# Optimization experiments

Measured on AMD Instinct MI355X. Metric: run time of the kernel, lower is better.

Reference implementation:

```python
import jax, jax.numpy as jnp
import numpy as np

B, C, N, Fd = 8, 64, 256, 128
EPS = 1e-5


def setup_inputs() -> dict:
    key = jax.random.key(0)
    k_h, k_op, k_s, k_q = jax.random.split(key, 4)
    # xavier_uniform bound for [C, 2F, 1] slices: gain*sqrt(6/(fan_in+fan_out)) with fan_in=2F, fan_out=1
    bound = float(np.sqrt(6.0 / (2 * Fd + 1)))
    h = jax.random.normal(k_h, (B, C, N, Fd), dtype=jnp.float32)
    op = jax.random.uniform(k_op, (C, 2 * Fd, 1), minval=-bound, maxval=bound, dtype=jnp.float32)
    op_S = jax.random.uniform(k_s, (C, 2 * Fd, 1), minval=-bound, maxval=bound, dtype=jnp.float32)
    op_Q = jax.random.uniform(k_q, (C, 2 * Fd, 1), minval=-bound, maxval=bound, dtype=jnp.float32)
    gamma = jnp.ones((C,), dtype=jnp.float32)
    beta = jnp.zeros((C,), dtype=jnp.float32)
    return {"h": h, "op": op, "op_S": op_S, "op_Q": op_Q, "gamma": gamma, "beta": beta}


def reference(h, op, op_S, op_Q, gamma, beta):
    # h: [B, C, N, F]
    source = h[:, :, 0:1, :]                              # [B,C,1,F]
    h_src = jnp.broadcast_to(source, h.shape)             # repeat_interleave over N
    h_op = jnp.concatenate([h_src, h], axis=-1)           # [B,C,N,2F]
    # [B,C,N,2F] x [C,2F,1] -> [B,C,N,1]
    attn_op = jax.nn.sigmoid(jnp.einsum('bcnf,cfo->bcno', h_op, op))
    op_mask = (attn_op >= 0.5).astype(h.dtype)            # hard threshold (no grad)
    supp = h * op_mask                                    # [B,C,N,F]
    query = h * (1.0 - op_mask)
    supp_mean = jnp.mean(supp, axis=2, keepdims=True)     # [B,C,1,F]
    query_mean = jnp.mean(query, axis=2, keepdims=True)
    supp_attn = jnp.einsum('bcnf,cfo->bcno', jnp.concatenate([supp_mean, source], axis=-1), op_S)
    query_attn = jnp.einsum('bcnf,cfo->bcno', jnp.concatenate([query_mean, source], axis=-1), op_Q)
    op_attn = jax.nn.softmax(jnp.concatenate([supp_attn, query_attn], axis=-1), axis=-1)  # [B,C,1,2]
    h_opn = supp * op_attn[..., 0:1] + query * op_attn[..., 1:2]  # [B,C,N,F]
    # BatchNorm2d (training-mode batch stats) over (B,N,F) per channel
    mean = jnp.mean(h_opn, axis=(0, 2, 3), keepdims=True)
    var = jnp.var(h_opn, axis=(0, 2, 3), keepdims=True)
    h_bn = (h_opn - mean) * jax.lax.rsqrt(var + EPS)
    h_bn = h_bn * gamma[None, :, None, None] + beta[None, :, None, None]
    return jax.nn.elu(h_bn)
```

## Files before the change

kernel.cpp:

```cpp
#include <hip/hip_runtime.h>
#include <math.h>

#define Bb 8
#define Cc 64
#define Nn 256
#define FD 128

__global__ __launch_bounds__(256) void k1(
    const float* __restrict__ h, const float* __restrict__ op,
    const float* __restrict__ opS, const float* __restrict__ opQ,
    float* __restrict__ w_out, float* __restrict__ partials) {
  const int bc = blockIdx.x;
  const int c = bc & (Cc - 1);
  const float* __restrict__ tile = h + (size_t)bc * (Nn * FD);

  __shared__ float s_ops[FD];
  __shared__ float s_oph[FD];
  __shared__ float s_dot[Nn];
  __shared__ float s_rs[Nn];
  __shared__ float s_rss[Nn];
  __shared__ float s_acc_s[8][FD];
  __shared__ float s_acc_q[8][FD];
  __shared__ float s_supp[FD];
  __shared__ float s_query[FD];
  __shared__ float s_scalar[8];
  __shared__ float s_wp[8];

  const int tid = threadIdx.x;
  const int lane = tid & 63;
  const int wv = tid >> 6;

  const float* __restrict__ opc  = op  + c * (2 * FD);
  const float* __restrict__ opSc = opS + c * (2 * FD);
  const float* __restrict__ opQc = opQ + c * (2 * FD);

  if (tid < FD) {
    s_ops[tid] = opc[tid];
    s_oph[tid] = opc[FD + tid];
  }
  __syncthreads();

  if (wv == 0) {
    float a = tile[lane], b2 = tile[lane + 64];
    float cs = a * s_ops[lane] + b2 * s_ops[lane + 64];
    float ss = a * opSc[FD + lane] + b2 * opSc[FD + lane + 64];
    float qq = a * opQc[FD + lane] + b2 * opQc[FD + lane + 64];
#pragma unroll
    for (int off = 32; off >= 1; off >>= 1) {
      cs += __shfl_xor(cs, off, 64);
      ss += __shfl_xor(ss, off, 64);
      qq += __shfl_xor(qq, off, 64);
    }
    if (lane == 0) { s_scalar[0] = cs; s_scalar[1] = ss; s_scalar[2] = qq; }
  }
  __syncthreads();
  const float const_src = s_scalar[0];

  {
    const int hl = lane & 31;
    const int rsel = lane >> 5;
    const float4 o4 = ((const float4*)s_oph)[hl];
#pragma unroll 4
    for (int i = 0; i < 32; ++i) {
      int n = wv * 64 + 2 * i + rsel;
      float4 v = ((const float4*)(tile + n * FD))[hl];
      float d   = v.x * o4.x + v.y * o4.y + v.z * o4.z + v.w * o4.w;
      float rs  = v.x + v.y + v.z + v.w;
      float rss = v.x * v.x + v.y * v.y + v.z * v.z + v.w * v.w;
#pragma unroll
      for (int off = 16; off >= 1; off >>= 1) {
        d   += __shfl_xor(d, off, 64);
        rs  += __shfl_xor(rs, off, 64);
        rss += __shfl_xor(rss, off, 64);
      }
      if (hl == 0) { s_dot[n] = d + const_src; s_rs[n] = rs; s_rss[n] = rss; }
    }
  }
  __syncthreads();

  {
    const int f4  = tid & 31;
    const int sub = (tid >> 5) & 3;
    const int g   = tid >> 7;
    const int slot = g * 4 + sub;
    float4 ssum = {0, 0, 0, 0}, qsum = {0, 0, 0, 0};
#pragma unroll 4
    for (int it = 0; it < 32; ++it) {
      int n = g * 128 + it * 4 + sub;
      float4 v = ((const float4*)(tile + n * FD))[f4];
      if (s_dot[n] >= 0.0f) {
        ssum.x += v.x; ssum.y += v.y; ssum.z += v.z; ssum.w += v.w;
      } else {
        qsum.x += v.x; qsum.y += v.y; qsum.z += v.z; qsum.w += v.w;
      }
    }
    ((float4*)s_acc_s[slot])[f4] = ssum;
    ((float4*)s_acc_q[slot])[f4] = qsum;
  }
  __syncthreads();
  if (tid < FD) {
    float v = 0;
#pragma unroll
    for (int k = 0; k < 8; ++k) v += s_acc_s[k][tid];
    s_supp[tid] = v;
  } else {
    int f = tid - FD;
    float v = 0;
#pragma unroll
    for (int k = 0; k < 8; ++k) v += s_acc_q[k][f];
    s_query[f] = v;
  }
  __syncthreads();

  if (wv == 0) {
    float sa = s_supp[lane] * opSc[lane] + s_supp[lane + 64] * opSc[lane + 64];
    float qa = s_query[lane] * opQc[lane] + s_query[lane + 64] * opQc[lane + 64];
#pragma unroll
    for (int off = 32; off >= 1; off >>= 1) {
      sa += __shfl_xor(sa, off, 64);
      qa += __shfl_xor(qa, off, 64);
    }
    if (lane == 0) {
      sa = sa * (1.0f / Nn) + s_scalar[1];
      qa = qa * (1.0f / Nn) + s_scalar[2];
      float mx = fmaxf(sa, qa);
      float es = expf(sa - mx), eq = expf(qa - mx);
      float inv = 1.0f / (es + eq);
      s_scalar[3] = es * inv;
      s_scalar[4] = eq * inv;
    }
  }
  __syncthreads();

  {
    const float wsup = s_scalar[3], wqry = s_scalar[4];
    const int n = tid;
    float wn = (s_dot[n] >= 0.0f) ? wsup : wqry;
    w_out[bc * Nn + n] = wn;
    float ps  = wn * s_rs[n];
    float pss = wn * wn * s_rss[n];
#pragma unroll
    for (int off = 32; off >= 1; off >>= 1) {
      ps  += __shfl_xor(ps, off, 64);
      pss += __shfl_xor(pss, off, 64);
    }
    if (lane == 0) { s_wp[wv] = ps; s_wp[4 + wv] = pss; }
  }
  __syncthreads();
  if (tid == 0) {
    float S  = s_wp[0] + s_wp[1] + s_wp[2] + s_wp[3];
    float SS = s_wp[4] + s_wp[5] + s_wp[6] + s_wp[7];
    partials[bc * 2]     = S;
    partials[bc * 2 + 1] = SS;
  }
}

__global__ __launch_bounds__(256) void k2(
    const float* __restrict__ h, const float* __restrict__ w_in,
    const float* __restrict__ partials, const float* __restrict__ gamma,
    const float* __restrict__ beta, float* __restrict__ out) {
  const int bc = blockIdx.x;
  const int c = bc & (Cc - 1);
  const int tid = threadIdx.x;
  __shared__ float s_w[Nn];
  __shared__ float s_sc[2];

  s_w[tid] = w_in[bc * Nn + tid];
  if (tid == 0) {
    float S = 0.0f, SS = 0.0f;
#pragma unroll
    for (int b2 = 0; b2 < Bb; ++b2) {
      S  += partials[(b2 * Cc + c) * 2];
      SS += partials[(b2 * Cc + c) * 2 + 1];
    }
    const float invcnt = 1.0f / (float)(Bb * Nn * FD);
    float mean = S * invcnt;
    float var  = SS * invcnt - mean * mean;
    float inv  = rsqrtf(var + 1e-5f);
    float g = gamma[c] * inv;
    s_sc[0] = g;
    s_sc[1] = beta[c] - mean * g;
  }
  __syncthreads();

  const float scale = s_sc[0], shift = s_sc[1];
  const float4* __restrict__ h4 = (const float4*)(h + (size_t)bc * (Nn * FD));
  float4* __restrict__ o4 = (float4*)(out + (size_t)bc * (Nn * FD));
#pragma unroll 4
  for (int i = tid; i < Nn * FD / 4; i += 256) {
    const float wn = s_w[i >> 5];
    float4 v = h4[i];
    float4 r;
    r.x = v.x * wn * scale + shift;
    r.y = v.y * wn * scale + shift;
    r.z = v.z * wn * scale + shift;
    r.w = v.w * wn * scale + shift;
    r.x = (r.x > 0.0f) ? r.x : expm1f(r.x);
    r.y = (r.y > 0.0f) ? r.y : expm1f(r.y);
    r.z = (r.z > 0.0f) ? r.z : expm1f(r.z);
    r.w = (r.w > 0.0f) ? r.w : expm1f(r.w);
    o4[i] = r;
  }
}

extern "C" void kernel_launch(void* const* d_in, const int* in_sizes, int n_in,
                              void* d_out, int out_size, void* d_ws, size_t ws_size,
                              hipStream_t stream) {
  const float* h     = (const float*)d_in[0];
  const float* op    = (const float*)d_in[1];
  const float* opS   = (const float*)d_in[2];
  const float* opQ   = (const float*)d_in[3];
  const float* gamma = (const float*)d_in[4];
  const float* beta  = (const float*)d_in[5];
  float* out = (float*)d_out;

  float* w_ws     = (float*)d_ws;
  float* partials = w_ws + Bb * Cc * Nn;

  k1<<<Bb * Cc, 256, 0, stream>>>(h, op, opS, opQ, w_ws, partials);
  k2<<<Bb * Cc, 256, 0, stream>>>(h, w_ws, partials, gamma, beta, out);
}
```

Measured before the change: 160.1 us.

## Single-pass stats via per-row dot products and split work across more blocks

Replaces the two-pass masked mean over h with an algebraic reformulation: per-row dot products with op_S and op_Q plus row sums are computed in one read, so the masked means and the batch-norm moments come from scalars instead of a second tile sweep. Work is split into four row segments per (b,c), which gives more blocks for the streaming passes. A small per-channel kernel combines the partials, and the final pass uses fast __expf. The cost is an extra launch and a different summation order, and __expf is less accurate than expm1f near zero.

New measurement: 144.3 us. 9.8% less time.

```diff
diff --git a/kernel.cpp b/kernel.cpp
--- a/kernel.cpp
+++ b/kernel.cpp
@@ -5,201 +5,174 @@
 #define Cc 64
 #define Nn 256
 #define FD 128
+#define SEGS 4
+#define ROWS 64
+#define TILE (Nn * FD)
 
-__global__ __launch_bounds__(256) void k1(
+__global__ __launch_bounds__(256) void s1(
     const float* __restrict__ h, const float* __restrict__ op,
     const float* __restrict__ opS, const float* __restrict__ opQ,
-    float* __restrict__ w_out, float* __restrict__ partials) {
-  const int bc = blockIdx.x;
+    unsigned long long* __restrict__ maskbuf, float* __restrict__ bpart) {
+  const int blk = blockIdx.x;
+  const int bc = blk >> 2, seg = blk & 3;
   const int c = bc & (Cc - 1);
-  const float* __restrict__ tile = h + (size_t)bc * (Nn * FD);
+  const float* __restrict__ tile = h + (size_t)bc * TILE;
+  const int tid = threadIdx.x, lane = tid & 63, wv = tid >> 6;
+  const int hw = tid >> 5, hl = tid & 31;
 
-  __shared__ float s_ops[FD];
-  __shared__ float s_oph[FD];
-  __shared__ float s_dot[Nn];
-  __shared__ float s_rs[Nn];
-  __shared__ float s_rss[Nn];
-  __shared__ float s_acc_s[8][FD];
-  __shared__ float s_acc_q[8][FD];
-  __shared__ float s_supp[FD];
-  __shared__ float s_query[FD];
-  __shared__ float s_scalar[8];
-  __shared__ float s_wp[8];
+  __shared__ float s_dh[ROWS], s_dS[ROWS], s_dQ[ROWS], s_rs[ROWS], s_rss[ROWS];
 
-  const int tid = threadIdx.x;
-  const int lane = tid & 63;
-  const int wv = tid >> 6;
+  float const_src = 0.0f;
+  if (wv == 0) {
+    const float* __restrict__ opc = op + c * 2 * FD;
+    float a = tile[lane], b = tile[lane + 64];
+    float cs = a * opc[lane] + b * opc[lane + 64];
+#pragma unroll
+    for (int off = 32; off >= 1; off >>= 1) cs += __shfl_xor(cs, off, 64);
+    const_src = cs;
+  }
 
-  const float* __restrict__ opc  = op  + c * (2 * FD);
-  const float* __restrict__ opSc = opS + c * (2 * FD);
-  const float* __restrict__ opQc = opQ + c * (2 * FD);
+  const float4 oH = ((const float4*)(op  + c * 2 * FD + FD))[hl];
+  const float4 oS = ((const float4*)(opS + c * 2 * FD))[hl];
+  const float4 oQ = ((const float4*)(opQ + c * 2 * FD))[hl];
 
-  if (tid < FD) {
-    s_ops[tid] = opc[tid];
-    s_oph[tid] = opc[FD + tid];
+#pragma unroll
+  for (int i = 0; i < 8; ++i) {
+    const int nl = hw * 8 + i;
+    const float4 v = ((const float4*)(tile + (size_t)(seg * ROWS + nl) * FD))[hl];
+    float dh  = v.x * oH.x + v.y * oH.y + v.z * oH.z + v.w * oH.w;
+    float ds  = v.x * oS.x + v.y * oS.y + v.z * oS.z + v.w * oS.w;
+    float dq  = v.x * oQ.x + v.y * oQ.y + v.z * oQ.z + v.w * oQ.w;
+    float rs  = v.x + v.y + v.z + v.w;
+    float rss = v.x * v.x + v.y * v.y + v.z * v.z + v.w * v.w;
+#pragma unroll
+    for (int off = 16; off >= 1; off >>= 1) {
+      dh  += __shfl_xor(dh,  off, 64);
+      ds  += __shfl_xor(ds,  off, 64);
+      dq  += __shfl_xor(dq,  off, 64);
+      rs  += __shfl_xor(rs,  off, 64);
+      rss += __shfl_xor(rss, off, 64);
+    }
+    if (hl == 0) {
+      s_dh[nl] = dh; s_dS[nl] = ds; s_dQ[nl] = dq; s_rs[nl] = rs; s_rss[nl] = rss;
+    }
   }
   __syncthreads();
 
   if (wv == 0) {
-    float a = tile[lane], b2 = tile[lane + 64];
-    float cs = a * s_ops[lane] + b2 * s_ops[lane + 64];
-    float ss = a * opSc[FD + lane] + b2 * opSc[FD + lane + 64];
-    float qq = a * opQc[FD + lane] + b2 * opQc[FD + lane + 64];
+    const int r = lane;
+    const bool m = (s_dh[r] + const_src) >= 0.0f;
+    const unsigned long long bits = __ballot(m);
+    float dsm  = m ? s_dS[r]  : 0.0f;
+    float dqq  = m ? 0.0f     : s_dQ[r];
+    float rsm  = m ? s_rs[r]  : 0.0f;
+    float rsq  = m ? 0.0f     : s_rs[r];
+    float rssm = m ? s_rss[r] : 0.0f;
+    float rssq = m ? 0.0f     : s_rss[r];
 #pragma unroll
     for (int off = 32; off >= 1; off >>= 1) {
-      cs += __shfl_xor(cs, off, 64);
-      ss += __shfl_xor(ss, off, 64);
-      qq += __shfl_xor(qq, off, 64);
+      dsm  += __shfl_xor(dsm,  off, 64);
+      dqq  += __shfl_xor(dqq,  off, 64);
+      rsm  += __shfl_xor(rsm,  off, 64);
+      rsq  += __shfl_xor(rsq,  off, 64);
+      rssm += __shfl_xor(rssm, off, 64);
+      rssq += __shfl_xor(rssq, off, 64);
     }
-    if (lane == 0) { s_scalar[0] = cs; s_scalar[1] = ss; s_scalar[2] = qq; }
-  }
-  __syncthreads();
-  const float const_src = s_scalar[0];
-
-  {
-    const int hl = lane & 31;
-    const int rsel = lane >> 5;
-    const float4 o4 = ((const float4*)s_oph)[hl];
-#pragma unroll 4
-    for (int i = 0; i < 32; ++i) {
-      int n = wv * 64 + 2 * i + rsel;
-      float4 v = ((const float4*)(tile + n * FD))[hl];
-      float d   = v.x * o4.x + v.y * o4.y + v.z * o4.z + v.w * o4.w;
-      float rs  = v.x + v.y + v.z + v.w;
-      float rss = v.x * v.x + v.y * v.y + v.z * v.z + v.w * v.w;
-#pragma unroll
-      for (int off = 16; off >= 1; off >>= 1) {
-        d   += __shfl_xor(d, off, 64);
-        rs  += __shfl_xor(rs, off, 64);
-        rss += __shfl_xor(rss, off, 64);
-      }
-      if (hl == 0) { s_dot[n] = d + const_src; s_rs[n] = rs; s_rss[n] = rss; }
+    if (lane == 0) {
+      float* p = bpart + blk * 8;
+      p[0] = dsm; p[1] = dqq; p[2] = rsm; p[3] = rsq; p[4] = rssm; p[5] = rssq;
+      maskbuf[blk] = bits;
     }
   }
-  __syncthreads();
+}
 
-  {
-    const int f4  = tid & 31;
-    const int sub = (tid >> 5) & 3;
-    const int g   = tid >> 7;
-    const int slot = g * 4 + sub;
-    float4 ssum = {0, 0, 0, 0}, qsum = {0, 0, 0, 0};
-#pragma unroll 4
-    for (int it = 0; it < 32; ++it) {
-      int n = g * 128 + it * 4 + sub;
-      float4 v = ((const float4*)(tile + n * FD))[f4];
-      if (s_dot[n] >= 0.0f) {
-        ssum.x += v.x; ssum.y += v.y; ssum.z += v.z; ssum.w += v.w;
-      } else {
-        qsum.x += v.x; qsum.y += v.y; qsum.z += v.z; qsum.w += v.w;
-      }
+__global__ __launch_bounds__(256) void s2(
+    const float* __restrict__ h, const float* __restrict__ opS,
+    const float* __restrict__ opQ, const float* __restrict__ bpart,
+    const float* __restrict__ gamma, const float* __restrict__ beta,
+    float* __restrict__ wsq, float* __restrict__ chan) {
+  const int c = blockIdx.x;
+  const int tid = threadIdx.x, lane = tid & 63, wv = tid >> 6, hl = tid & 31;
+  const int b = wv * 2 + ((lane >> 5) & 1);
+  __shared__ float s_S[Bb], s_SS[Bb];
+
+  const int bc = b * Cc + c;
+  const float4 s4 = ((const float4*)(h + (size_t)bc * TILE))[hl];
+  const float4 oS = ((const float4*)(opS + c * 2 * FD + FD))[hl];
+  const float4 oQ = ((const float4*)(opQ + c * 2 * FD + FD))[hl];
+  float ss = s4.x * oS.x + s4.y * oS.y + s4.z * oS.z + s4.w * oS.w;
+  float qq = s4.x * oQ.x + s4.y * oQ.y + s4.z * oQ.z + s4.w * oQ.w;
+#pragma unroll
+  for (int off = 16; off >= 1; off >>= 1) {
+    ss += __shfl_xor(ss, off, 64);
+    qq += __shfl_xor(qq, off, 64);
+  }
+
+  if (hl == 0) {
+    float a0 = 0, a1 = 0, a2 = 0, a3 = 0, a4 = 0, a5 = 0;
+#pragma unroll
+    for (int k = 0; k < SEGS; ++k) {
+      const float* p = bpart + (size_t)(bc * SEGS + k) * 8;
+      a0 += p[0]; a1 += p[1]; a2 += p[2]; a3 += p[3]; a4 += p[4]; a5 += p[5];
     }
-    ((float4*)s_acc_s[slot])[f4] = ssum;
-    ((float4*)s_acc_q[slot])[f4] = qsum;
-  }
-  __syncthreads();
-  if (tid < FD) {
-    float v = 0;
-#pragma unroll
-    for (int k = 0; k < 8; ++k) v += s_acc_s[k][tid];
-    s_supp[tid] = v;
-  } else {
-    int f = tid - FD;
-    float v = 0;
-#pragma unroll
-    for (int k = 0; k < 8; ++k) v += s_acc_q[k][f];
-    s_query[f] = v;
-  }
-  __syncthreads();
-
-  if (wv == 0) {
-    float sa = s_supp[lane] * opSc[lane] + s_supp[lane + 64] * opSc[lane + 64];
-    float qa = s_query[lane] * opQc[lane] + s_query[lane + 64] * opQc[lane + 64];
-#pragma unroll
-    for (int off = 32; off >= 1; off >>= 1) {
-      sa += __shfl_xor(sa, off, 64);
-      qa += __shfl_xor(qa, off, 64);
-    }
-    if (lane == 0) {
-      sa = sa * (1.0f / Nn) + s_scalar[1];
-      qa = qa * (1.0f / Nn) + s_scalar[2];
-      float mx = fmaxf(sa, qa);
-      float es = expf(sa - mx), eq = expf(qa - mx);
-      float inv = 1.0f / (es + eq);
-      s_scalar[3] = es * inv;
-      s_scalar[4] = eq * inv;
-    }
-  }
-  __syncthreads();
-
-  {
-    const float wsup = s_scalar[3], wqry = s_scalar[4];
-    const int n = tid;
-    float wn = (s_dot[n] >= 0.0f) ? wsup : wqry;
-    w_out[bc * Nn + n] = wn;
-    float ps  = wn * s_rs[n];
-    float pss = wn * wn * s_rss[n];
-#pragma unroll
-    for (int off = 32; off >= 1; off >>= 1) {
-      ps  += __shfl_xor(ps, off, 64);
-      pss += __shfl_xor(pss, off, 64);
-    }
-    if (lane == 0) { s_wp[wv] = ps; s_wp[4 + wv] = pss; }
+    float sa = a0 * (1.0f / Nn) + ss;
+    float qa = a1 * (1.0f / Nn) + qq;
+    float mx = fmaxf(sa, qa);
+    float es = __expf(sa - mx), eq = __expf(qa - mx);
+    float inv = 1.0f / (es + eq);
+    float w_s = es * inv, w_q = eq * inv;
+    wsq[bc * 2] = w_s;
+    wsq[bc * 2 + 1] = w_q;
+    s_S[b]  = w_s * a2 + w_q * a3;
+    s_SS[b] = w_s * w_s * a4 + w_q * w_q * a5;
   }
   __syncthreads();
   if (tid == 0) {
-    float S  = s_wp[0] + s_wp[1] + s_wp[2] + s_wp[3];
-    float SS = s_wp[4] + s_wp[5] + s_wp[6] + s_wp[7];
-    partials[bc * 2]     = S;
-    partials[bc * 2 + 1] = SS;
+    float S = 0, SS = 0;
+#pragma unroll
+    for (int k = 0; k < Bb; ++k) { S += s_S[k]; SS += s_SS[k]; }
+    const float invcnt = 1.0f / (float)(Bb * Nn * FD);
+    float mean = S * invcnt;
+    float var = SS * invcnt - mean * mean;
+    float sc = gamma[c] * rsqrtf(var + 1e-5f);
+    chan[c * 2] = sc;
+    chan[c * 2 + 1] = beta[c] - mean * sc;
   }
 }
 
-__global__ __launch_bounds__(256) void k2(
-    const float* __restrict__ h, const float* __restrict__ w_in,
-    const float* __restrict__ partials, const float* __restrict__ gamma,
-    const float* __restrict__ beta, float* __restrict__ out) {
-  const int bc = blockIdx.x;
-  const int c = bc & (Cc - 1);
+__global__ __launch_bounds__(256) void s3(
+    const float* __restrict__ h, const unsigned long long* __restrict__ maskbuf,
+    const float* __restrict__ wsq, const float* __restrict__ chan,
+    float* __restrict__ out) {
+  const int blk = blockIdx.x, bc = blk >> 2, seg = blk & 3, c = bc & (Cc - 1);
   const int tid = threadIdx.x;
-  __shared__ float s_w[Nn];
-  __shared__ float s_sc[2];
-
-  s_w[tid] = w_in[bc * Nn + tid];
-  if (tid == 0) {
-    float S = 0.0f, SS = 0.0f;
-#pragma unroll
-    for (int b2 = 0; b2 < Bb; ++b2) {
-      S  += partials[(b2 * Cc + c) * 2];
-      SS += partials[(b2 * Cc + c) * 2 + 1];
-    }
-    const float invcnt = 1.0f / (float)(Bb * Nn * FD);
-    float mean = S * invcnt;
-    float var  = SS * invcnt - mean * mean;
-    float inv  = rsqrtf(var + 1e-5f);
-    float g = gamma[c] * inv;
-    s_sc[0] = g;
-    s_sc[1] = beta[c] - mean * g;
+  __shared__ float s_a[ROWS];
+  __shared__ float s_shift;
+  if (tid < ROWS) {
+    const unsigned long long m = maskbuf[blk];
+    const float w = ((m >> tid) & 1ull) ? wsq[bc * 2] : wsq[bc * 2 + 1];
+    s_a[tid] = w * chan[c * 2];
+    if (tid == 0) s_shift = chan[c * 2 + 1];
   }
   __syncthreads();
-
-  const float scale = s_sc[0], shift = s_sc[1];
-  const float4* __restrict__ h4 = (const float4*)(h + (size_t)bc * (Nn * FD));
-  float4* __restrict__ o4 = (float4*)(out + (size_t)bc * (Nn * FD));
-#pragma unroll 4
-  for (int i = tid; i < Nn * FD / 4; i += 256) {
-    const float wn = s_w[i >> 5];
-    float4 v = h4[i];
+  const float shift = s_shift;
+  const float4* __restrict__ h4 = (const float4*)(h + (size_t)bc * TILE) + seg * 2048;
+  float4* __restrict__ o4 = (float4*)(out + (size_t)bc * TILE) + seg * 2048;
+#pragma unroll
+  for (int k = 0; k < 8; ++k) {
+    const int idx = k * 256 + tid;
+    const float a = s_a[idx >> 5];
+    float4 v = h4[idx];
     float4 r;
-    r.x = v.x * wn * scale + shift;
-    r.y = v.y * wn * scale + shift;
-    r.z = v.z * wn * scale + shift;
-    r.w = v.w * wn * scale + shift;
-    r.x = (r.x > 0.0f) ? r.x : expm1f(r.x);
-    r.y = (r.y > 0.0f) ? r.y : expm1f(r.y);
-    r.z = (r.z > 0.0f) ? r.z : expm1f(r.z);
-    r.w = (r.w > 0.0f) ? r.w : expm1f(r.w);
-    o4[i] = r;
+    r.x = fmaf(v.x, a, shift);
+    r.y = fmaf(v.y, a, shift);
+    r.z = fmaf(v.z, a, shift);
+    r.w = fmaf(v.w, a, shift);
+    r.x = r.x > 0.0f ? r.x : __expf(r.x) - 1.0f;
+    r.y = r.y > 0.0f ? r.y : __expf(r.y) - 1.0f;
+    r.z = r.z > 0.0f ? r.z : __expf(r.z) - 1.0f;
+    r.w = r.w > 0.0f ? r.w : __expf(r.w) - 1.0f;
+    o4[idx] = r;
   }
 }
 
@@ -214,9 +187,12 @@
   const float* beta  = (const float*)d_in[5];
   float* out = (float*)d_out;
 
-  float* w_ws     = (float*)d_ws;
-  float* partials = w_ws + Bb * Cc * Nn;
+  unsigned long long* maskbuf = (unsigned long long*)d_ws;
+  float* bpart = (float*)((char*)d_ws + 16384);
+  float* wsq   = (float*)((char*)d_ws + 16384 + 65536);
+  float* chan  = (float*)((char*)d_ws + 16384 + 65536 + 4096);
 
-  k1<<<Bb * Cc, 256, 0, stream>>>(h, op, opS, opQ, w_ws, partials);
-  k2<<<Bb * Cc, 256, 0, stream>>>(h, w_ws, partials, gamma, beta, out);
+  s1<<<Bb * Cc * SEGS, 256, 0, stream>>>(h, op, opS, opQ, maskbuf, bpart);
+  s2<<<Cc, 256, 0, stream>>>(h, opS, opQ, bpart, gamma, beta, wsq, chan);
+  s3<<<Bb * Cc * SEGS, 256, 0, stream>>>(h, maskbuf, wsq, chan, out);
 }
```
